# Performance work log

Measured on AMD Instinct MI355X. Metric: run time of the kernel, lower is better.

Reference implementation:

```python
import jax, jax.numpy as jnp
import numpy as np

NUM_CLASSES = 151  # Visual Genome object classes
PRED_DIM = 51      # predicate distribution channels (50 predicates + bg)


def _conv2d(x, w, pad):
    # x: [B, Cin, H, W], w: [Cout, Cin, kh, kw]
    return jax.lax.conv_general_dilated(
        x, w, window_strides=(1, 1), padding=[(pad, pad), (pad, pad)],
        dimension_numbers=("NCHW", "OIHW", "NCHW"))


def setup_inputs() -> dict:
    key = jax.random.key(0)
    ks = jax.random.split(key, 12)
    B, N, D = 64, 80, 4096
    K = D // 4  # 1024
    s = 0.02
    return {
        "encoder_reps": jax.random.normal(ks[0], (B, N, D), jnp.float32),
        "obj_preds": jax.random.randint(ks[1], (B, N), 0, NUM_CLASSES, jnp.int32),
        "freq_table": jax.random.normal(ks[2], (NUM_CLASSES * NUM_CLASSES, PRED_DIM), jnp.float32),
        "W_comp": jax.random.normal(ks[3], (D, K), jnp.float32) * s,
        "W_ou1": jax.random.normal(ks[4], (K, K), jnp.float32) * s,
        "W_ofc": jax.random.normal(ks[5], (K, K), jnp.float32) * s,
        "W_decomp": jax.random.normal(ks[6], (K, D), jnp.float32) * s,
        "conv1": jax.random.normal(ks[7], (10, PRED_DIM, 3, 3), jnp.float32) * s,
        "conv2": jax.random.normal(ks[8], (5, 10, 3, 3), jnp.float32) * s,
        "conv3": jax.random.normal(ks[9], (1, 5, 1, 1), jnp.float32) * s,
    }


def reference(encoder_reps, obj_preds, freq_table, W_comp, W_ou1, W_ofc,
              W_decomp, conv1, conv2, conv3):
    B, N, D = encoder_reps.shape
    # obj_comp: Linear(D, D//4, bias=False) + ReLU
    comp = jax.nn.relu(jnp.einsum("bnd,dk->bnk", encoder_reps, W_comp))  # [B,N,K]
    # ou1: Linear(K, K, bias=False) + ReLU
    obj_u1 = jax.nn.relu(jnp.einsum("bnk,kj->bnj", comp, W_ou1))          # [B,N,K]
    # pairwise product indices -> freq_bias.index_with_labels (subj*C + obj)
    pair_idx = obj_preds[:, :, None] * NUM_CLASSES + obj_preds[:, None, :]  # [B,N,N]
    rel_u1 = freq_table[pair_idx]                                          # [B,N,N,51]
    # adjacency via small conv stack + sigmoid
    x = jnp.transpose(rel_u1, (0, 3, 1, 2))      # [B,51,N,N]
    x = _conv2d(x, conv1, pad=1)                 # [B,10,N,N]
    x = _conv2d(x, conv2, pad=1)                 # [B,5,N,N]
    x = _conv2d(x, conv3, pad=0)                 # [B,1,N,N]
    adj = jax.nn.sigmoid(x[:, 0])                # [B,N,N]
    # normalized Laplacian: D^-1/2 (A + I) D^-1/2
    A_hat = adj + jnp.eye(N, dtype=adj.dtype)[None]
    d = (jnp.sum(A_hat, axis=2) + 1e-5) ** (-0.5)                          # [B,N]
    L_hat = d[:, :, None] * A_hat * d[:, None, :]                          # [B,N,N]
    ofl_u = jnp.einsum("bnm,bmk->bnk", L_hat, obj_u1)                      # [B,N,K]
    # ofc_u + obj_decomp + residual
    u_m = jax.nn.relu(jnp.einsum("bnk,kj->bnj", ofl_u, W_ofc))
    decomp = jax.nn.relu(jnp.einsum("bnk,kd->bnd", u_m, W_decomp))
    return decomp + encoder_reps
```

## Files before the change

kernel.cpp:

```cpp
#include <hip/hip_runtime.h>
#include <hip/hip_bf16.h>
#include <math.h>

typedef __bf16 bf16x8 __attribute__((ext_vector_type(8)));
typedef float floatx4 __attribute__((ext_vector_type(4)));
typedef float float4v __attribute__((ext_vector_type(4)));
typedef float float2v __attribute__((ext_vector_type(2)));
typedef unsigned short ushortx4 __attribute__((ext_vector_type(4)));
typedef unsigned short ushortx8 __attribute__((ext_vector_type(8)));

__device__ __forceinline__ unsigned short f2bf(float f) {
    unsigned int u = __builtin_bit_cast(unsigned int, f);
    u += 0x7FFFu + ((u >> 16) & 1u);
    return (unsigned short)(u >> 16);
}
__device__ __forceinline__ float bf2f(unsigned short h) {
    unsigned int u = ((unsigned int)h) << 16;
    return __builtin_bit_cast(float, u);
}

__device__ __forceinline__ void gload_lds16(const void* g, void* l) {
    __builtin_amdgcn_global_load_lds(
        (const __attribute__((address_space(1))) unsigned int*)g,
        (__attribute__((address_space(3))) unsigned int*)l, 16, 0, 0);
}

__global__ __launch_bounds__(256) void cast_bf16_kernel(
    const float* __restrict__ in, unsigned short* __restrict__ out, long n8)
{
    long i = (long)blockIdx.x * 256 + threadIdx.x;
    long stride = (long)gridDim.x * 256;
    for (; i < n8; i += stride) {
        float4v a = reinterpret_cast<const float4v*>(in)[2 * i];
        float4v b = reinterpret_cast<const float4v*>(in)[2 * i + 1];
        ushortx8 h;
        #pragma unroll
        for (int q = 0; q < 4; ++q) { h[q] = f2bf(a[q]); h[4 + q] = f2bf(b[q]); }
        reinterpret_cast<ushortx8*>(out)[i] = h;
    }
}

__global__ __launch_bounds__(256) void reduce_relu_kernel(
    const unsigned short* __restrict__ p, unsigned short* __restrict__ out,
    long n8, long half_elems)
{
    long i = (long)blockIdx.x * 256 + threadIdx.x;
    long stride = (long)gridDim.x * 256;
    const ushortx8* p0 = reinterpret_cast<const ushortx8*>(p);
    const ushortx8* p1 = reinterpret_cast<const ushortx8*>(p + half_elems);
    for (; i < n8; i += stride) {
        ushortx8 a = p0[i], b = p1[i];
        ushortx8 h;
        #pragma unroll
        for (int q = 0; q < 8; ++q)
            h[q] = f2bf(fmaxf(bf2f(a[q]) + bf2f(b[q]), 0.0f));
        reinterpret_cast<ushortx8*>(out)[i] = h;
    }
}

__global__ __launch_bounds__(256) void prep_kernel(
    const float* __restrict__ w1, const float* __restrict__ w2,
    const float* __restrict__ w3, float* __restrict__ W1e,
    float* __restrict__ w23)
{
    for (int idx = threadIdx.x; idx < 4590; idx += 256) {
        int ci = idx / 90, rem = idx % 90;
        int tap = rem / 10, co = rem % 10;
        int di = tap / 3, dj = tap % 3;
        W1e[idx] = w1[((co * 51 + ci) * 3 + di) * 3 + dj];
    }
    if (threadIdx.x < 90) {
        int tap = threadIdx.x / 10, c10 = threadIdx.x % 10;
        int di = tap / 3, dj = tap % 3;
        float s = 0.f;
        #pragma unroll
        for (int c5 = 0; c5 < 5; ++c5)
            s = fmaf(w3[c5], w2[((c5 * 10 + c10) * 3 + di) * 3 + dj], s);
        w23[threadIdx.x] = s;
    }
}

__global__ __launch_bounds__(256) void fp1_kernel(
    const float* __restrict__ freq, const float* __restrict__ W1e,
    float* __restrict__ Fp1)
{
    __shared__ float W1s[4590];
    for (int idx = threadIdx.x; idx < 4590; idx += 256)
        W1s[idx] = W1e[idx];
    __syncthreads();
    int p = blockIdx.x * 256 + threadIdx.x;
    if (p >= 22801) return;
    float2v acc[45];
    #pragma unroll
    for (int t = 0; t < 45; ++t) { acc[t][0] = 0.f; acc[t][1] = 0.f; }
    const float* fr = freq + (size_t)p * 51;
    for (int ci = 0; ci < 51; ++ci) {
        float v = fr[ci];
        const float2v* wrow = reinterpret_cast<const float2v*>(&W1s[ci * 90]);
        #pragma unroll
        for (int t = 0; t < 45; ++t) {
            float2v w = wrow[t];
            acc[t][0] = fmaf(v, w[0], acc[t][0]);
            acc[t][1] = fmaf(v, w[1], acc[t][1]);
        }
    }
    float2v* out = reinterpret_cast<float2v*>(Fp1 + (size_t)p * 90);
    #pragma unroll
    for (int t = 0; t < 45; ++t) out[t] = acc[t];
}

__global__ __launch_bounds__(320) void gather_kernel(
    const int* __restrict__ preds, const float* __restrict__ Fp1,
    float* __restrict__ h1)
{
    __shared__ int pb[80];
    const int b = blockIdx.y;
    const int tid = threadIdx.x;
    if (tid < 80) pb[tid] = preds[b * 80 + tid];
    __syncthreads();
    const int i = blockIdx.x * 4 + tid / 80;
    const int j = tid % 80;
    float2v acc[5];
    #pragma unroll
    for (int q = 0; q < 5; ++q) { acc[q][0] = 0.f; acc[q][1] = 0.f; }
    #pragma unroll
    for (int di = 0; di < 3; ++di) {
        int ii = i + di - 1;
        if (ii < 0 || ii >= 80) continue;
        int pi = pb[ii] * 151;
        #pragma unroll
        for (int dj = 0; dj < 3; ++dj) {
            int jj = j + dj - 1;
            if (jj < 0 || jj >= 80) continue;
            const float2v* row = reinterpret_cast<const float2v*>(
                Fp1 + (size_t)(pi + pb[jj]) * 90 + (di * 3 + dj) * 10);
            #pragma unroll
            for (int q = 0; q < 5; ++q) {
                float2v v = row[q];
                acc[q][0] += v[0];
                acc[q][1] += v[1];
            }
        }
    }
    float2v* out = reinterpret_cast<float2v*>(
        h1 + ((size_t)b * 6400 + i * 80 + j) * 10);
    #pragma unroll
    for (int q = 0; q < 5; ++q) out[q] = acc[q];
}

__global__ __launch_bounds__(320) void conv23_kernel(
    const float* __restrict__ h1, const float* __restrict__ w23g,
    float* __restrict__ adj)
{
    __shared__ float w23s[90];
    const int tid = threadIdx.x;
    if (tid < 90) w23s[tid] = w23g[tid];
    __syncthreads();
    const int b = blockIdx.y;
    const int i = blockIdx.x * 4 + tid / 80;
    const int j = tid % 80;
    float t = 0.f;
    #pragma unroll
    for (int di = 0; di < 3; ++di) {
        int ii = i + di - 1;
        if (ii < 0 || ii >= 80) continue;
        #pragma unroll
        for (int dj = 0; dj < 3; ++dj) {
            int jj = j + dj - 1;
            if (jj < 0 || jj >= 80) continue;
            const float2v* hp = reinterpret_cast<const float2v*>(
                h1 + ((size_t)b * 6400 + ii * 80 + jj) * 10);
            const float* wp = w23s + (di * 3 + dj) * 10;
            #pragma unroll
            for (int q = 0; q < 5; ++q) {
                float2v v = hp[q];
                t = fmaf(v[0], wp[2 * q], t);
                t = fmaf(v[1], wp[2 * q + 1], t);
            }
        }
    }
    adj[(size_t)b * 6400 + i * 80 + j] = 1.0f / (1.0f + __expf(-t));
}

__global__ __launch_bounds__(128) void degree_kernel(
    const float* __restrict__ adj, float* __restrict__ deg)
{
    int b = blockIdx.x;
    int i = threadIdx.x;
    if (i >= 80) return;
    const float* row = adj + (size_t)b * 6400 + i * 80;
    float s = 1.0f + 1e-5f;
    for (int jj = 0; jj < 80; ++jj) s += row[jj];
    deg[b * 80 + i] = rsqrtf(s);
}

__global__ __launch_bounds__(256) void transpose_cast(
    const float* __restrict__ in, unsigned short* __restrict__ out,
    int R, int C)
{
    __shared__ float t[32][33];
    const int tx = threadIdx.x & 31;
    const int ty = threadIdx.x >> 5;
    const int r0 = blockIdx.y * 32, c0 = blockIdx.x * 32;
    #pragma unroll
    for (int k = 0; k < 4; ++k)
        t[ty + k * 8][tx] = in[(size_t)(r0 + ty + k * 8) * C + c0 + tx];
    __syncthreads();
    #pragma unroll
    for (int k = 0; k < 4; ++k)
        out[(size_t)(c0 + ty + k * 8) * R + r0 + tx] = f2bf(t[tx][ty + k * 8]);
}

template<bool A_BF16, int MODE>
__global__ __launch_bounds__(256) void gemm_mfma(
    const void* __restrict__ Ap, const unsigned short* __restrict__ Bt,
    void* __restrict__ Cp, const float* __restrict__ Rp,
    int M, int N, int lda, int kh)
{
    constexpr int LDA = A_BF16 ? 32 : 40;
    __shared__ unsigned short Al[2][128 * LDA];
    __shared__ unsigned short Bl[2][128 * 32];

    const int tid  = threadIdx.x;
    const int bm   = blockIdx.x * 128;
    const int bn   = blockIdx.y * 128;
    const int zoff = blockIdx.z * kh;
    const int wave = tid >> 6;
    const int lane = tid & 63;
    const int wm   = (wave >> 1) * 64;
    const int wn   = (wave & 1) * 64;
    const int lr   = lane & 15;
    const int lk   = (lane >> 4) * 8;

    floatx4 acc[4][4];
    #pragma unroll
    for (int i = 0; i < 4; ++i)
        #pragma unroll
        for (int j = 0; j < 4; ++j)
            #pragma unroll
            for (int r = 0; r < 4; ++r) acc[i][j][r] = 0.0f;

    auto stage = [&](int buf, int k0) {
        if constexpr (A_BF16) {
            const unsigned short* A = (const unsigned short*)Ap;
            #pragma unroll
            for (int it = 0; it < 2; ++it) {
                int idx = tid + it * 256;
                int r = idx >> 2, kc = (idx & 3) * 8;
                gload_lds16(&A[(size_t)(bm + r) * lda + k0 + kc],
                            &Al[buf][idx * 8]);
            }
        } else {
            const float* A = (const float*)Ap;
            #pragma unroll
            for (int it = 0; it < 4; ++it) {
                int idx = tid + it * 256;
                int r = idx >> 3, kc = (idx & 7) * 4;
                float4v v = *reinterpret_cast<const float4v*>(
                    &A[(size_t)(bm + r) * lda + k0 + kc]);
                ushortx4 h;
                #pragma unroll
                for (int q = 0; q < 4; ++q) h[q] = f2bf(v[q]);
                *reinterpret_cast<ushortx4*>(&Al[buf][r * 40 + kc]) = h;
            }
        }
        #pragma unroll
        for (int it = 0; it < 2; ++it) {
            int idx = tid + it * 256;
            int r = idx >> 2, kc = (idx & 3) * 8;
            gload_lds16(&Bt[(size_t)(bn + r) * lda + k0 + kc],
                        &Bl[buf][idx * 8]);
        }
    };

    stage(0, zoff);
    __syncthreads();

    const int nt = kh >> 5;
    int cur = 0;
    for (int t = 0; t < nt; ++t) {
        if (t + 1 < nt) stage(cur ^ 1, zoff + ((t + 1) << 5));

        bf16x8 af[4], bfv[4];
        #pragma unroll
        for (int mi = 0; mi < 4; ++mi)
            af[mi] = *reinterpret_cast<const bf16x8*>(
                &Al[cur][(wm + mi * 16 + lr) * LDA + lk]);
        #pragma unroll
        for (int ni = 0; ni < 4; ++ni)
            bfv[ni] = *reinterpret_cast<const bf16x8*>(
                &Bl[cur][(wn + ni * 16 + lr) * 32 + lk]);
        #pragma unroll
        for (int mi = 0; mi < 4; ++mi)
            #pragma unroll
            for (int ni = 0; ni < 4; ++ni)
                acc[mi][ni] = __builtin_amdgcn_mfma_f32_16x16x32_bf16(
                    af[mi], bfv[ni], acc[mi][ni], 0, 0, 0);

        __syncthreads();
        cur ^= 1;
    }

    #pragma unroll
    for (int mi = 0; mi < 4; ++mi) {
        #pragma unroll
        for (int ni = 0; ni < 4; ++ni) {
            #pragma unroll
            for (int r = 0; r < 4; ++r) {
                int row = bm + wm + mi * 16 + (lane >> 4) * 4 + r;
                int col = bn + wn + ni * 16 + lr;
                size_t off = (size_t)row * N + col;
                if (MODE == 0) {
                    ((unsigned short*)Cp)[off] = f2bf(fmaxf(acc[mi][ni][r], 0.f));
                } else if (MODE == 1) {
                    ((float*)Cp)[off] = fmaxf(acc[mi][ni][r], 0.f) + Rp[off];
                } else {
                    ((unsigned short*)Cp)[(size_t)blockIdx.z * M * N + off] =
                        f2bf(acc[mi][ni][r]);
                }
            }
        }
    }
}

__global__ __launch_bounds__(256) void laplacian_kernel(
    const float* __restrict__ adj, const float* __restrict__ deg,
    const unsigned short* __restrict__ u_in, unsigned short* __restrict__ ofl)
{
    __shared__ float wl[6400];
    __shared__ unsigned short ul[80 * 256];
    const int b   = blockIdx.y;
    const int kq  = blockIdx.x;
    const int tid = threadIdx.x;
    const int ko  = tid & 31;
    const int ngrp = tid >> 5;

    const float* ab = adj + (size_t)b * 6400;
    const float* db = deg + b * 80;
    for (int idx = tid; idx < 6400; idx += 256) {
        int n = idx / 80;
        int m = idx - n * 80;
        float w = ab[idx] + (n == m ? 1.0f : 0.0f);
        wl[idx] = w * db[m];
    }
    const unsigned short* ub = u_in + (size_t)b * 80 * 1024 + kq * 256;
    #pragma unroll
    for (int it = 0; it < 10; ++it) {
        int idx = tid + it * 256;
        int m   = idx >> 5;
        int c8  = (idx & 31) * 8;
        *reinterpret_cast<ushortx8*>(&ul[m * 256 + c8]) =
            *reinterpret_cast<const ushortx8*>(&ub[(size_t)m * 1024 + c8]);
    }
    __syncthreads();

    float acc[10][8];
    #pragma unroll
    for (int ni = 0; ni < 10; ++ni)
        #pragma unroll
        for (int q = 0; q < 8; ++q) acc[ni][q] = 0.0f;

    for (int m = 0; m < 80; ++m) {
        ushortx8 uv = *reinterpret_cast<const ushortx8*>(&ul[m * 256 + ko * 8]);
        float uf[8];
        #pragma unroll
        for (int q = 0; q < 8; ++q) uf[q] = bf2f(uv[q]);
        #pragma unroll
        for (int ni = 0; ni < 10; ++ni) {
            float wv = wl[(ngrp * 10 + ni) * 80 + m];
            #pragma unroll
            for (int q = 0; q < 8; ++q)
                acc[ni][q] = fmaf(wv, uf[q], acc[ni][q]);
        }
    }
    #pragma unroll
    for (int ni = 0; ni < 10; ++ni) {
        int n = ngrp * 10 + ni;
        float dn = db[n];
        ushortx8 o;
        #pragma unroll
        for (int q = 0; q < 8; ++q) o[q] = f2bf(acc[ni][q] * dn);
        *reinterpret_cast<ushortx8*>(
            &ofl[((size_t)(b * 80 + n)) * 1024 + kq * 256 + ko * 8]) = o;
    }
}

extern "C" void kernel_launch(void* const* d_in, const int* in_sizes, int n_in,
                              void* d_out, int out_size, void* d_ws, size_t ws_size,
                              hipStream_t stream)
{
    const float* enc   = (const float*)d_in[0];
    const int*   preds = (const int*)d_in[1];
    const float* freq  = (const float*)d_in[2];
    const float* Wc    = (const float*)d_in[3];
    const float* Wou1  = (const float*)d_in[4];
    const float* Wofc  = (const float*)d_in[5];
    const float* Wdec  = (const float*)d_in[6];
    const float* w1    = (const float*)d_in[7];
    const float* w2    = (const float*)d_in[8];
    const float* w3    = (const float*)d_in[9];

    const int M = 5120;
    unsigned short* comp  = (unsigned short*)d_ws;
    unsigned short* obju  = comp + (size_t)M * 1024;
    unsigned short* r1    = obju + (size_t)M * 1024;
    unsigned short* oflu  = r1;
    float*          h1    = (float*)r1;
    unsigned short* P     = r1;
    unsigned short* r2    = r1 + 8192000;
    unsigned short* um    = r2;
    float*          Fp1   = (float*)r2;
    unsigned short* Wcb   = r2 + (size_t)M * 1024;
    unsigned short* Wou1b = Wcb + (size_t)1024 * 4096;
    unsigned short* Wofcb = Wou1b + (size_t)1024 * 1024;
    unsigned short* Wdecb = Wofcb + (size_t)1024 * 1024;
    float*          W1e   = (float*)(Wdecb + (size_t)4096 * 1024);
    float*          w23   = W1e + 4590;
    float*          adj   = w23 + 90;
    float*          deg   = adj + (size_t)64 * 6400;
    unsigned short* encb  = (unsigned short*)(deg + 5120);
    const size_t need_bytes =
        ((size_t)(encb - comp) + (size_t)M * 4096) * sizeof(unsigned short);
    const bool use_encb = ws_size >= need_bytes;

    prep_kernel<<<1, 256, 0, stream>>>(w1, w2, w3, W1e, w23);
    transpose_cast<<<dim3(32, 128), 256, 0, stream>>>(Wc, Wcb, 4096, 1024);
    transpose_cast<<<dim3(32, 32), 256, 0, stream>>>(Wou1, Wou1b, 1024, 1024);
    transpose_cast<<<dim3(32, 32), 256, 0, stream>>>(Wofc, Wofcb, 1024, 1024);
    transpose_cast<<<dim3(128, 32), 256, 0, stream>>>(Wdec, Wdecb, 1024, 4096);

    fp1_kernel<<<90, 256, 0, stream>>>(freq, W1e, Fp1);
    gather_kernel<<<dim3(20, 64), 320, 0, stream>>>(preds, Fp1, h1);
    conv23_kernel<<<dim3(20, 64), 320, 0, stream>>>(h1, w23, adj);
    degree_kernel<<<64, 128, 0, stream>>>(adj, deg);

    if (use_encb) {
        cast_bf16_kernel<<<2048, 256, 0, stream>>>(
            enc, encb, (long)M * 4096 / 8);
        gemm_mfma<true, 2><<<dim3(40, 8, 2), 256, 0, stream>>>(
            encb, Wcb, P, nullptr, M, 1024, 4096, 2048);
        reduce_relu_kernel<<<2048, 256, 0, stream>>>(
            P, comp, (long)M * 1024 / 8, (size_t)M * 1024);
    } else {
        gemm_mfma<false, 0><<<dim3(40, 8), 256, 0, stream>>>(
            enc, Wcb, comp, nullptr, M, 1024, 4096, 4096);
    }
    gemm_mfma<true, 0><<<dim3(40, 8), 256, 0, stream>>>(
        comp, Wou1b, obju, nullptr, M, 1024, 1024, 1024);
    laplacian_kernel<<<dim3(4, 64), 256, 0, stream>>>(adj, deg, obju, oflu);
    gemm_mfma<true, 0><<<dim3(40, 8), 256, 0, stream>>>(
        oflu, Wofcb, um, nullptr, M, 1024, 1024, 1024);
    gemm_mfma<true, 1><<<dim3(40, 32), 256, 0, stream>>>(
        um, Wdecb, d_out, enc, M, 4096, 1024, 1024);
}
```

Baseline: 347.1 us.

## Triple-buffer bf16 GEMM with async LDS loads and XOR-swizzled shared layout

The bf16-A GEMM now keeps three LDS stages and prefetches two k-tiles ahead. It uses a vmcnt wait plus one barrier per iteration in place of two syncthreads, so the global-to-LDS loads overlap more with the MFMA work. The k-chunk offsets are XOR-swizzled by row on both the async copy and the fragment reads, to cut LDS bank conflicts without padding. The fp32-A path is split into its own kernel that keeps the old double-buffered scheme. The tradeoffs are more LDS per block, which may lower occupancy, and a hand-tuned wait count that must match the number of outstanding loads.

```diff
diff --git a/kernel.cpp b/kernel.cpp
--- a/kernel.cpp
+++ b/kernel.cpp
@@ -211,15 +211,14 @@
         out[(size_t)(c0 + ty + k * 8) * R + r0 + tx] = f2bf(t[tx][ty + k * 8]);
 }
 
-template<bool A_BF16, int MODE>
-__global__ __launch_bounds__(256) void gemm_mfma(
-    const void* __restrict__ Ap, const unsigned short* __restrict__ Bt,
+template<int MODE>
+__global__ __launch_bounds__(256) void gemm_pipe(
+    const unsigned short* __restrict__ Ap, const unsigned short* __restrict__ Bt,
     void* __restrict__ Cp, const float* __restrict__ Rp,
     int M, int N, int lda, int kh)
 {
-    constexpr int LDA = A_BF16 ? 32 : 40;
-    __shared__ unsigned short Al[2][128 * LDA];
-    __shared__ unsigned short Bl[2][128 * 32];
+    __shared__ unsigned short Al[3][128 * 32];
+    __shared__ unsigned short Bl[3][128 * 32];
 
     const int tid  = threadIdx.x;
     const int bm   = blockIdx.x * 128;
@@ -231,6 +230,7 @@
     const int wn   = (wave & 1) * 64;
     const int lr   = lane & 15;
     const int lk   = (lane >> 4) * 8;
+    const int lkz  = lk ^ ((lr & 1) << 3) ^ (((lr >> 1) & 1) << 4);
 
     floatx4 acc[4][4];
     #pragma unroll
@@ -241,64 +241,54 @@
             for (int r = 0; r < 4; ++r) acc[i][j][r] = 0.0f;
 
     auto stage = [&](int buf, int k0) {
-        if constexpr (A_BF16) {
-            const unsigned short* A = (const unsigned short*)Ap;
-            #pragma unroll
-            for (int it = 0; it < 2; ++it) {
-                int idx = tid + it * 256;
-                int r = idx >> 2, kc = (idx & 3) * 8;
-                gload_lds16(&A[(size_t)(bm + r) * lda + k0 + kc],
-                            &Al[buf][idx * 8]);
-            }
-        } else {
-            const float* A = (const float*)Ap;
-            #pragma unroll
-            for (int it = 0; it < 4; ++it) {
-                int idx = tid + it * 256;
-                int r = idx >> 3, kc = (idx & 7) * 4;
-                float4v v = *reinterpret_cast<const float4v*>(
-                    &A[(size_t)(bm + r) * lda + k0 + kc]);
-                ushortx4 h;
-                #pragma unroll
-                for (int q = 0; q < 4; ++q) h[q] = f2bf(v[q]);
-                *reinterpret_cast<ushortx4*>(&Al[buf][r * 40 + kc]) = h;
-            }
-        }
         #pragma unroll
         for (int it = 0; it < 2; ++it) {
             int idx = tid + it * 256;
             int r = idx >> 2, kc = (idx & 3) * 8;
-            gload_lds16(&Bt[(size_t)(bn + r) * lda + k0 + kc],
+            int kcz = kc ^ ((r & 1) << 3) ^ (((r >> 1) & 1) << 4);
+            gload_lds16(&Ap[(size_t)(bm + r) * lda + k0 + kcz],
+                        &Al[buf][idx * 8]);
+        }
+        #pragma unroll
+        for (int it = 0; it < 2; ++it) {
+            int idx = tid + it * 256;
+            int r = idx >> 2, kc = (idx & 3) * 8;
+            int kcz = kc ^ ((r & 1) << 3) ^ (((r >> 1) & 1) << 4);
+            gload_lds16(&Bt[(size_t)(bn + r) * lda + k0 + kcz],
                         &Bl[buf][idx * 8]);
         }
     };
 
+    const int nt = kh >> 5;
     stage(0, zoff);
-    __syncthreads();
-
-    const int nt = kh >> 5;
-    int cur = 0;
+    if (nt > 1) stage(1, zoff + 32);
+
     for (int t = 0; t < nt; ++t) {
-        if (t + 1 < nt) stage(cur ^ 1, zoff + ((t + 1) << 5));
-
+        if (t < nt - 1) {
+            asm volatile("s_waitcnt vmcnt(4)" ::: "memory");
+        } else {
+            asm volatile("s_waitcnt vmcnt(0)" ::: "memory");
+        }
+        __builtin_amdgcn_s_barrier();
+        __builtin_amdgcn_sched_barrier(0);
+        if (t + 2 < nt) stage((t + 2) % 3, zoff + ((t + 2) << 5));
+
+        const int cur = t % 3;
         bf16x8 af[4], bfv[4];
         #pragma unroll
         for (int mi = 0; mi < 4; ++mi)
             af[mi] = *reinterpret_cast<const bf16x8*>(
-                &Al[cur][(wm + mi * 16 + lr) * LDA + lk]);
+                &Al[cur][(wm + mi * 16 + lr) * 32 + lkz]);
         #pragma unroll
         for (int ni = 0; ni < 4; ++ni)
             bfv[ni] = *reinterpret_cast<const bf16x8*>(
-                &Bl[cur][(wn + ni * 16 + lr) * 32 + lk]);
+                &Bl[cur][(wn + ni * 16 + lr) * 32 + lkz]);
         #pragma unroll
         for (int mi = 0; mi < 4; ++mi)
             #pragma unroll
             for (int ni = 0; ni < 4; ++ni)
                 acc[mi][ni] = __builtin_amdgcn_mfma_f32_16x16x32_bf16(
                     af[mi], bfv[ni], acc[mi][ni], 0, 0, 0);
-
-        __syncthreads();
-        cur ^= 1;
     }
 
     #pragma unroll
@@ -321,6 +311,85 @@
             }
         }
     }
+}
+
+__global__ __launch_bounds__(256) void gemm_f32a(
+    const float* __restrict__ Ap, const unsigned short* __restrict__ Bt,
+    unsigned short* __restrict__ Cp, int M, int N, int lda)
+{
+    __shared__ unsigned short Al[2][128 * 40];
+    __shared__ unsigned short Bl[2][128 * 32];
+    const int tid  = threadIdx.x;
+    const int bm   = blockIdx.x * 128;
+    const int bn   = blockIdx.y * 128;
+    const int wave = tid >> 6;
+    const int lane = tid & 63;
+    const int wm   = (wave >> 1) * 64;
+    const int wn   = (wave & 1) * 64;
+    const int lr   = lane & 15;
+    const int lk   = (lane >> 4) * 8;
+
+    floatx4 acc[4][4];
+    #pragma unroll
+    for (int i = 0; i < 4; ++i)
+        #pragma unroll
+        for (int j = 0; j < 4; ++j)
+            #pragma unroll
+            for (int r = 0; r < 4; ++r) acc[i][j][r] = 0.0f;
+
+    auto stage = [&](int buf, int k0) {
+        #pragma unroll
+        for (int it = 0; it < 4; ++it) {
+            int idx = tid + it * 256;
+            int r = idx >> 3, kc = (idx & 7) * 4;
+            float4v v = *reinterpret_cast<const float4v*>(
+                &Ap[(size_t)(bm + r) * lda + k0 + kc]);
+            ushortx4 h;
+            #pragma unroll
+            for (int q = 0; q < 4; ++q) h[q] = f2bf(v[q]);
+            *reinterpret_cast<ushortx4*>(&Al[buf][r * 40 + kc]) = h;
+        }
+        #pragma unroll
+        for (int it = 0; it < 2; ++it) {
+            int idx = tid + it * 256;
+            gload_lds16(&Bt[(size_t)(bn + (idx >> 2)) * lda + k0 + (idx & 3) * 8],
+                        &Bl[buf][idx * 8]);
+        }
+    };
+    stage(0, 0);
+    __syncthreads();
+    const int nt = lda >> 5;
+    int cur = 0;
+    for (int t = 0; t < nt; ++t) {
+        if (t + 1 < nt) stage(cur ^ 1, (t + 1) << 5);
+        bf16x8 af[4], bfv[4];
+        #pragma unroll
+        for (int mi = 0; mi < 4; ++mi)
+            af[mi] = *reinterpret_cast<const bf16x8*>(
+                &Al[cur][(wm + mi * 16 + lr) * 40 + lk]);
+        #pragma unroll
+        for (int ni = 0; ni < 4; ++ni)
+            bfv[ni] = *reinterpret_cast<const bf16x8*>(
+                &Bl[cur][(wn + ni * 16 + lr) * 32 + lk]);
+        #pragma unroll
+        for (int mi = 0; mi < 4; ++mi)
+            #pragma unroll
+            for (int ni = 0; ni < 4; ++ni)
+                acc[mi][ni] = __builtin_amdgcn_mfma_f32_16x16x32_bf16(
+                    af[mi], bfv[ni], acc[mi][ni], 0, 0, 0);
+        __syncthreads();
+        cur ^= 1;
+    }
+    #pragma unroll
+    for (int mi = 0; mi < 4; ++mi)
+        #pragma unroll
+        for (int ni = 0; ni < 4; ++ni)
+            #pragma unroll
+            for (int r = 0; r < 4; ++r) {
+                int row = bm + wm + mi * 16 + (lane >> 4) * 4 + r;
+                int col = bn + wn + ni * 16 + lr;
+                Cp[(size_t)row * N + col] = f2bf(fmaxf(acc[mi][ni][r], 0.f));
+            }
 }
 
 __global__ __launch_bounds__(256) void laplacian_kernel(
@@ -437,19 +506,19 @@
     if (use_encb) {
         cast_bf16_kernel<<<2048, 256, 0, stream>>>(
             enc, encb, (long)M * 4096 / 8);
-        gemm_mfma<true, 2><<<dim3(40, 8, 2), 256, 0, stream>>>(
+        gemm_pipe<2><<<dim3(40, 8, 2), 256, 0, stream>>>(
             encb, Wcb, P, nullptr, M, 1024, 4096, 2048);
         reduce_relu_kernel<<<2048, 256, 0, stream>>>(
             P, comp, (long)M * 1024 / 8, (size_t)M * 1024);
     } else {
-        gemm_mfma<false, 0><<<dim3(40, 8), 256, 0, stream>>>(
-            enc, Wcb, comp, nullptr, M, 1024, 4096, 4096);
-    }
-    gemm_mfma<true, 0><<<dim3(40, 8), 256, 0, stream>>>(
+        gemm_f32a<<<dim3(40, 8), 256, 0, stream>>>(
+            enc, Wcb, comp, M, 1024, 4096);
+    }
+    gemm_pipe<0><<<dim3(40, 8), 256, 0, stream>>>(
         comp, Wou1b, obju, nullptr, M, 1024, 1024, 1024);
     laplacian_kernel<<<dim3(4, 64), 256, 0, stream>>>(adj, deg, obju, oflu);
-    gemm_mfma<true, 0><<<dim3(40, 8), 256, 0, stream>>>(
+    gemm_pipe<0><<<dim3(40, 8), 256, 0, stream>>>(
         oflu, Wofcb, um, nullptr, M, 1024, 1024, 1024);
-    gemm_mfma<true, 1><<<dim3(40, 32), 256, 0, stream>>>(
+    gemm_pipe<1><<<dim3(40, 32), 256, 0, stream>>>(
         um, Wdecb, d_out, enc, M, 4096, 1024, 1024);
 }
```

Result: no change. 349.2 us (+0.6%).
